# Kernel tuning notes

Measured on AMD Instinct MI355X. Metric: run time of the kernel, lower is better.

The kernel has to match this reference:

```python
import jax, jax.numpy as jnp
import numpy as np

EPS = 1e-5
NUM_GROUPS = 32

def _nin(x, w, b):
    # 1x1 conv: x (B,C,H,W), w (K,C), b (K,)
    return jnp.einsum('bchw,kc->bkhw', x, w) + b[None, :, None, None]

def _group_norm(x, gamma, beta, num_groups=NUM_GROUPS, eps=EPS):
    B, C, H, W = x.shape
    xg = x.reshape(B, num_groups, C // num_groups, H, W)
    mean = xg.mean(axis=(2, 3, 4), keepdims=True)
    var = xg.var(axis=(2, 3, 4), keepdims=True)
    xg = (xg - mean) * jax.lax.rsqrt(var + eps)
    x = xg.reshape(B, C, H, W)
    return x * gamma[None, :, None, None] + beta[None, :, None, None]

def setup_inputs() -> dict:
    key = jax.random.key(0)
    ks = jax.random.split(key, 10)
    B, C, H, W = 8, 512, 64, 64
    att = 512
    s = 0.02
    return {
        'x': jax.random.normal(ks[0], (B, C, H, W), dtype=jnp.float32),
        'gn_weight': jnp.ones((C,), jnp.float32),
        'gn_bias': jnp.zeros((C,), jnp.float32),
        'q_w': jax.random.normal(ks[1], (att, C), jnp.float32) * s,
        'q_b': jnp.zeros((att,), jnp.float32),
        'k_w': jax.random.normal(ks[2], (att, C), jnp.float32) * s,
        'k_b': jnp.zeros((att,), jnp.float32),
        'v_w': jax.random.normal(ks[3], (att, C), jnp.float32) * s,
        'v_b': jnp.zeros((att,), jnp.float32),
        'proj_w': jax.random.normal(ks[4], (C, att), jnp.float32) * s,
        'proj_b': jnp.zeros((C,), jnp.float32),
    }

def reference(x, gn_weight, gn_bias, q_w, q_b, k_w, k_b, v_w, v_b, proj_w, proj_b):
    B, C, H, W = x.shape
    h = _group_norm(x, gn_weight, gn_bias)
    q = _nin(h, q_w, q_b)  # (B, D, H, W)
    k = _nin(h, k_w, k_b)
    v = _nin(h, v_w, v_b)
    N = H * W
    qf = q.reshape(B, -1, N)
    kf = k.reshape(B, -1, N)
    vf = v.reshape(B, -1, N)
    scale = C ** (-0.5)  # note: scaled by input channel C, per source
    w = jnp.einsum('bdn,bdm->bnm', qf, kf) * scale  # (B, N, N)
    w = jax.nn.softmax(w, axis=-1)
    hf = jnp.einsum('bnm,bdm->bdn', w, vf)
    h = hf.reshape(B, -1, H, W)
    h = _nin(h, proj_w, proj_b)
    return x + h
```

## Files before the change

kernel.cpp:

```cpp
#include <hip/hip_runtime.h>
#include <hip/hip_bf16.h>
#include <cstdint>
#include <cstddef>

typedef __bf16 bf16_t;
typedef __bf16 bf16x8 __attribute__((ext_vector_type(8)));
typedef __bf16 bf16x4 __attribute__((ext_vector_type(4)));
typedef float f32x4 __attribute__((ext_vector_type(4)));

__device__ __forceinline__ void async16(const void* g, void* l) {
  __builtin_amdgcn_global_load_lds(
      (const __attribute__((address_space(1))) void*)g,
      (__attribute__((address_space(3))) void*)l,
      16, 0, 0);
}

__global__ __launch_bounds__(256) void f2b4(const float* __restrict__ w0,
                                            const float* __restrict__ w1,
                                            const float* __restrict__ w2,
                                            const float* __restrict__ w3,
                                            bf16_t* __restrict__ o0,
                                            bf16_t* __restrict__ o1,
                                            bf16_t* __restrict__ o2,
                                            bf16_t* __restrict__ o3) {
  const float* in = (blockIdx.y == 0) ? w0 : (blockIdx.y == 1) ? w1
                   : (blockIdx.y == 2) ? w2 : w3;
  bf16_t* out = (blockIdx.y == 0) ? o0 : (blockIdx.y == 1) ? o1
               : (blockIdx.y == 2) ? o2 : o3;
  const int i = blockIdx.x * 256 + threadIdx.x;
  float4 v = ((const float4*)in)[i];
  bf16x4 o = { (__bf16)v.x, (__bf16)v.y, (__bf16)v.z, (__bf16)v.w };
  ((bf16x4*)out)[i] = o;
}

__global__ __launch_bounds__(256) void groupnorm_t(const float* __restrict__ x,
                                                   const float* __restrict__ gamma,
                                                   const float* __restrict__ beta,
                                                   bf16_t* __restrict__ ht) {
  const int g = blockIdx.x;
  const int b = blockIdx.y;
  const int t = threadIdx.x;
  const float* xg = x + ((size_t)(b * 512 + g * 16)) * 4096;
  const float4* x4 = (const float4*)xg;

  float s = 0.f, ss = 0.f;
  #pragma unroll 8
  for (int i = t; i < 16384; i += 256) {
    float4 v = x4[i];
    s  += (v.x + v.y) + (v.z + v.w);
    ss += (v.x * v.x + v.y * v.y) + (v.z * v.z + v.w * v.w);
  }
  #pragma unroll
  for (int o = 32; o; o >>= 1) { s += __shfl_xor(s, o); ss += __shfl_xor(ss, o); }
  __shared__ float rs[4], rss[4];
  if ((t & 63) == 0) { rs[t >> 6] = s; rss[t >> 6] = ss; }
  __syncthreads();
  const float S  = (rs[0] + rs[1]) + (rs[2] + rs[3]);
  const float SS = (rss[0] + rss[1]) + (rss[2] + rss[3]);
  const float inv_n = 1.0f / 65536.0f;
  const float mean = S * inv_n;
  const float var  = SS * inv_n - mean * mean;
  const float rstd = rsqrtf(var + 1e-5f);

  float ga[16], be[16];
  #pragma unroll
  for (int cc = 0; cc < 16; cc++) {
    const float gm = gamma[g * 16 + cc] * rstd;
    ga[cc] = gm;
    be[cc] = beta[g * 16 + cc] - mean * gm;
  }

  bf16_t* hg = ht + (size_t)b * 4096 * 512 + g * 16;
  for (int n = t; n < 4096; n += 256) {
    bf16_t o[16];
    #pragma unroll
    for (int cc = 0; cc < 16; cc++)
      o[cc] = (bf16_t)(xg[(size_t)cc * 4096 + n] * ga[cc] + be[cc]);
    bf16x8* dst = (bf16x8*)(hg + (size_t)n * 512);
    dst[0] = *(bf16x8*)&o[0];
    dst[1] = *(bf16x8*)&o[8];
  }
}

template <int OUTF32, int BIAS_MODE, int RESID, int SWAP>
__global__ __launch_bounds__(256)
void gemm_bt(const bf16_t* __restrict__ A, const bf16_t* __restrict__ B,
             void* __restrict__ Cv, const float* __restrict__ bias,
             const float* __restrict__ resid,
             int TM, int TN, int Z, int K, float scale,
             long sA, long sB, long sC, long sR) {
  __shared__ alignas(16) bf16_t lA[4096];
  __shared__ alignas(16) bf16_t lB[4096];

  const int lid = blockIdx.x;
  const int xcd = lid & 7;
  const int j   = lid >> 3;
  const int sd  = SWAP ? TN : TM;
  const int I   = SWAP ? TM : TN;
  const int spx = (sd * Z) >> 3;
  const int strip = xcd * spx + j / I;
  const int inner = j % I;
  const int z    = strip / sd;
  const int sidx = strip % sd;
  const int bm = (SWAP ? inner : sidx) * 128;
  const int bn = (SWAP ? sidx : inner) * 128;
  const int N = TN * 128;

  const int t = threadIdx.x;
  const int lane = t & 63;
  const int w = t >> 6;
  const int wm = (w >> 1) * 64;
  const int wn = (w & 1) * 64;
  const bf16_t* Ab = A + (size_t)z * (size_t)sA;
  const bf16_t* Bb = B + (size_t)z * (size_t)sB;

  const int lrow = lane >> 2;
  const int lcol = (lane & 3) * 8;
  const int quad = lane >> 4;
  const int l15 = lane & 15;

  const bf16_t* gA0 = Ab + (size_t)(bm + w * 16 + lrow) * K + lcol;
  const bf16_t* gA1 = Ab + (size_t)(bm + (w + 4) * 16 + lrow) * K + lcol;
  const bf16_t* gB0 = Bb + (size_t)(bn + w * 16 + lrow) * K + lcol;
  const bf16_t* gB1 = Bb + (size_t)(bn + (w + 4) * 16 + lrow) * K + lcol;
  bf16_t* lA0 = &lA[w * 512];
  bf16_t* lA1 = &lA[(w + 4) * 512];
  bf16_t* lB0 = &lB[w * 512];
  bf16_t* lB1 = &lB[(w + 4) * 512];

  f32x4 acc[4][4] = {};

  for (int k0 = 0; k0 < K; k0 += 32) {
    __syncthreads();
    async16(gA0 + k0, lA0);
    async16(gA1 + k0, lA1);
    async16(gB0 + k0, lB0);
    async16(gB1 + k0, lB1);
    __syncthreads();

    bf16x8 af[4], bfr[4];
    #pragma unroll
    for (int i = 0; i < 4; i++) {
      af[i]  = *(const bf16x8*)&lA[(wm + i * 16 + l15) * 32 + quad * 8];
      bfr[i] = *(const bf16x8*)&lB[(wn + i * 16 + l15) * 32 + quad * 8];
    }
    #pragma unroll
    for (int i = 0; i < 4; i++)
      #pragma unroll
      for (int jj = 0; jj < 4; jj++)
        acc[i][jj] = __builtin_amdgcn_mfma_f32_16x16x32_bf16(af[i], bfr[jj],
                                                             acc[i][jj], 0, 0, 0);
  }

  float* Cf = (float*)Cv + (size_t)z * (size_t)sC;
  bf16_t* Cb = (bf16_t*)Cv + (size_t)z * (size_t)sC;
  const float* Rb = RESID ? (resid + (size_t)z * (size_t)sR) : nullptr;

  #pragma unroll
  for (int i = 0; i < 4; i++) {
    const int row0 = bm + wm + i * 16 + quad * 4;
    #pragma unroll
    for (int jj = 0; jj < 4; jj++) {
      const int col = bn + wn + jj * 16 + l15;
      #pragma unroll
      for (int r = 0; r < 4; r++) {
        float v = acc[i][jj][r] * scale;
        const int row = row0 + r;
        if (BIAS_MODE == 1) v += bias[row];
        else if (BIAS_MODE == 2) v += bias[col];
        const size_t idx = (size_t)row * N + col;
        if (RESID) v += Rb[idx];
        if (OUTF32) Cf[idx] = v;
        else Cb[idx] = (bf16_t)v;
      }
    }
  }
}

__global__ __launch_bounds__(512, 2)
void flash_attn(const bf16_t* __restrict__ Qm, const bf16_t* __restrict__ Km,
                const bf16_t* __restrict__ Vm, bf16_t* __restrict__ Om,
                float scale) {
  __shared__ alignas(16) bf16_t lT[2][4][128][32];
  __shared__ alignas(16) bf16_t lS[8][16][144];

  const int bid = blockIdx.x;
  const int z = bid & 7;
  const int qb = bid >> 3;
  const int m0 = qb * 128;

  const int t = threadIdx.x;
  const int lane = t & 63;
  const int w = t >> 6;
  const int quad = lane >> 4;
  const int l15 = lane & 15;
  const int srow = lane >> 2;
  const int scol = (lane & 3) * 8;

  const size_t sND = 4096ull * 512;
  const bf16_t* q = Qm + z * sND;
  const bf16_t* k = Km + z * sND;
  const bf16_t* v = Vm + z * sND;

  const bf16_t* kStage = k + (size_t)(w * 16 + srow) * 512 + scol;
  const bf16_t* vStage = v + (size_t)(w * 16 + srow) * 4096 + scol;

  bf16x8 qf[16];
  {
    const bf16_t* qrow = q + (size_t)(m0 + w * 16 + l15) * 512 + quad * 8;
    #pragma unroll
    for (int kk = 0; kk < 16; kk++)
      qf[kk] = *(const bf16x8*)(qrow + kk * 32);
  }

  f32x4 o_acc[32] = {};
  float l_run[4] = {0.f, 0.f, 0.f, 0.f};
  f32x4 s_acc[8];

  auto stageA = [&](int BUF, int kcc, int kd2) __attribute__((always_inline)) {
    #pragma unroll
    for (int c = 0; c < 4; c++)
      async16(kStage + (size_t)kcc * 512 + kd2 * 128 + c * 32,
              &lT[BUF][c][w * 16][0]);
  };
  auto stageC = [&](int BUF, int kcc, int db) __attribute__((always_inline)) {
    #pragma unroll
    for (int c = 0; c < 4; c++)
      async16(vStage + (size_t)db * 128 * 4096 + kcc + c * 32,
              &lT[BUF][c][w * 16][0]);
  };
  auto computeA = [&](int BUF, int kd2) __attribute__((always_inline)) {
    #pragma unroll
    for (int p = 0; p < 4; p++)
      #pragma unroll
      for (int n = 0; n < 8; n++) {
        bf16x8 kf = *(const bf16x8*)&lT[BUF][p][n * 16 + l15][quad * 8];
        s_acc[n] = __builtin_amdgcn_mfma_f32_16x16x32_bf16(
            qf[kd2 * 4 + p], kf, s_acc[n], 0, 0, 0);
      }
  };
  auto computeC = [&](int BUF, int db) __attribute__((always_inline)) {
    #pragma unroll
    for (int p = 0; p < 4; p++) {
      bf16x8 af = *(const bf16x8*)&lS[w][l15][p * 32 + quad * 8];
      #pragma unroll
      for (int nd = 0; nd < 8; nd++) {
        bf16x8 vf = *(const bf16x8*)&lT[BUF][p][nd * 16 + l15][quad * 8];
        o_acc[db * 8 + nd] = __builtin_amdgcn_mfma_f32_16x16x32_bf16(
            af, vf, o_acc[db * 8 + nd], 0, 0, 0);
      }
    }
  };
  auto phaseB = [&]() __attribute__((always_inline)) {
    float lsum[4] = {0.f, 0.f, 0.f, 0.f};
    #pragma unroll
    for (int n = 0; n < 8; n++)
      #pragma unroll
      for (int r = 0; r < 4; r++) {
        float e = __expf(s_acc[n][r] * scale);
        lsum[r] += e;
        lS[w][quad * 4 + r][n * 16 + l15] = (bf16_t)e;
      }
    #pragma unroll
    for (int r = 0; r < 4; r++) {
      float s = lsum[r];
      s += __shfl_xor(s, 1); s += __shfl_xor(s, 2);
      s += __shfl_xor(s, 4); s += __shfl_xor(s, 8);
      l_run[r] += s;
    }
  };

  stageA(0, 0, 0);
  __syncthreads();

  for (int kc = 0; kc < 4096; kc += 128) {
    #pragma unroll
    for (int n = 0; n < 8; n++) s_acc[n] = (f32x4){0.f, 0.f, 0.f, 0.f};

    stageA(1, kc, 1);  computeA(0, 0);            __syncthreads();
    stageA(0, kc, 2);  computeA(1, 1);            __syncthreads();
    stageA(1, kc, 3);  computeA(0, 2);            __syncthreads();
    stageC(0, kc, 0);  computeA(1, 3);  phaseB(); __syncthreads();
    stageC(1, kc, 1);  computeC(0, 0);            __syncthreads();
    stageC(0, kc, 2);  computeC(1, 1);            __syncthreads();
    stageC(1, kc, 3);  computeC(0, 2);            __syncthreads();
    if (kc + 128 < 4096) stageA(0, kc + 128, 0);
    computeC(1, 3);                               __syncthreads();
  }

  bf16_t* o = Om + z * sND;
  float rl[4];
  #pragma unroll
  for (int r = 0; r < 4; r++) rl[r] = 1.0f / l_run[r];
  #pragma unroll
  for (int nd = 0; nd < 32; nd++)
    #pragma unroll
    for (int r = 0; r < 4; r++) {
      const int row = m0 + w * 16 + quad * 4 + r;
      const int col = nd * 16 + l15;
      o[(size_t)row * 512 + col] = (bf16_t)(o_acc[nd][r] * rl[r]);
    }
}

extern "C" void kernel_launch(void* const* d_in, const int* in_sizes, int n_in,
                              void* d_out, int out_size, void* d_ws, size_t ws_size,
                              hipStream_t stream) {
  const float* x   = (const float*)d_in[0];
  const float* gnw = (const float*)d_in[1];
  const float* gnb = (const float*)d_in[2];
  const float* qw  = (const float*)d_in[3];
  const float* qb  = (const float*)d_in[4];
  const float* kw  = (const float*)d_in[5];
  const float* kb  = (const float*)d_in[6];
  const float* vw  = (const float*)d_in[7];
  const float* vb  = (const float*)d_in[8];
  const float* pw  = (const float*)d_in[9];
  const float* pb  = (const float*)d_in[10];
  float* out = (float*)d_out;

  char* ws = (char*)d_ws;
  size_t off = 0;
  auto alloc = [&](size_t bytes) -> void* {
    void* p = ws + off;
    off += (bytes + 255) & ~(size_t)255;
    return p;
  };

  const long sND = 4096L * 512;

  bf16_t* wqb = (bf16_t*)alloc(512ull * 512 * 2);
  bf16_t* wkb = (bf16_t*)alloc(512ull * 512 * 2);
  bf16_t* wvb = (bf16_t*)alloc(512ull * 512 * 2);
  bf16_t* wpb = (bf16_t*)alloc(512ull * 512 * 2);
  bf16_t* ht  = (bf16_t*)alloc(8ull * 4096 * 512 * 2);
  bf16_t* qbf = (bf16_t*)alloc(8ull * 4096 * 512 * 2);
  bf16_t* kbf = (bf16_t*)alloc(8ull * 4096 * 512 * 2);
  bf16_t* vbf = (bf16_t*)alloc(8ull * 4096 * 512 * 2);
  bf16_t* hfb = ht;

  f2b4<<<dim3(256, 4), 256, 0, stream>>>(qw, kw, vw, pw, wqb, wkb, wvb, wpb);
  groupnorm_t<<<dim3(32, 8), 256, 0, stream>>>(x, gnw, gnb, ht);

  gemm_bt<0, 2, 0, 0><<<1024, 256, 0, stream>>>(
      ht, wqb, qbf, qb, nullptr, 32, 4, 8, 512, 1.0f, sND, 0, sND, 0);
  gemm_bt<0, 2, 0, 0><<<1024, 256, 0, stream>>>(
      ht, wkb, kbf, kb, nullptr, 32, 4, 8, 512, 1.0f, sND, 0, sND, 0);
  gemm_bt<0, 1, 0, 1><<<1024, 256, 0, stream>>>(
      wvb, ht, vbf, vb, nullptr, 4, 32, 8, 512, 1.0f, 0, sND, sND, 0);

  const float scale = 0.044194173824159216f;
  flash_attn<<<256, 512, 0, stream>>>(qbf, kbf, vbf, hfb, scale);

  gemm_bt<1, 1, 1, 1><<<1024, 256, 0, stream>>>(
      wpb, hfb, out, pb, x, 4, 32, 8, 512, 1.0f, 0, sND, 512L * 4096, 512L * 4096);
}
```

Before: 701.8 us.

## Triple-buffer flash attention K/V staging with prefetch distance two and setprio

The LDS staging buffer grows from two to three slots so async global-to-LDS loads run two stages ahead of compute. Each stage now waits with a partial vmcnt plus a raw barrier instead of a full __syncthreads. The loop is unrolled in groups of three chunks so buffer indices stay compile-time constants. MFMA sections are also wrapped in s_setprio to favour math waves. The cost is more LDS per block, which may reduce occupancy, and fragile hand-counted vmcnt ordering.

```diff
diff --git a/kernel.cpp b/kernel.cpp
--- a/kernel.cpp
+++ b/kernel.cpp
@@ -181,7 +181,7 @@
 void flash_attn(const bf16_t* __restrict__ Qm, const bf16_t* __restrict__ Km,
                 const bf16_t* __restrict__ Vm, bf16_t* __restrict__ Om,
                 float scale) {
-  __shared__ alignas(16) bf16_t lT[2][4][128][32];
+  __shared__ alignas(16) bf16_t lT[3][4][128][32];
   __shared__ alignas(16) bf16_t lS[8][16][144];
 
   const int bid = blockIdx.x;
@@ -212,6 +212,7 @@
     for (int kk = 0; kk < 16; kk++)
       qf[kk] = *(const bf16x8*)(qrow + kk * 32);
   }
+  asm volatile("s_waitcnt vmcnt(0)" ::: "memory");
 
   f32x4 o_acc[32] = {};
   float l_run[4] = {0.f, 0.f, 0.f, 0.f};
@@ -230,6 +231,7 @@
               &lT[BUF][c][w * 16][0]);
   };
   auto computeA = [&](int BUF, int kd2) __attribute__((always_inline)) {
+    __builtin_amdgcn_s_setprio(1);
     #pragma unroll
     for (int p = 0; p < 4; p++)
       #pragma unroll
@@ -238,8 +240,10 @@
         s_acc[n] = __builtin_amdgcn_mfma_f32_16x16x32_bf16(
             qf[kd2 * 4 + p], kf, s_acc[n], 0, 0, 0);
       }
+    __builtin_amdgcn_s_setprio(0);
   };
   auto computeC = [&](int BUF, int db) __attribute__((always_inline)) {
+    __builtin_amdgcn_s_setprio(1);
     #pragma unroll
     for (int p = 0; p < 4; p++) {
       bf16x8 af = *(const bf16x8*)&lS[w][l15][p * 32 + quad * 8];
@@ -250,6 +254,7 @@
             af, vf, o_acc[db * 8 + nd], 0, 0, 0);
       }
     }
+    __builtin_amdgcn_s_setprio(0);
   };
   auto phaseB = [&]() __attribute__((always_inline)) {
     float lsum[4] = {0.f, 0.f, 0.f, 0.f};
@@ -269,24 +274,48 @@
       l_run[r] += s;
     }
   };
+  auto slotWB = [&]() __attribute__((always_inline)) {
+    asm volatile("s_waitcnt vmcnt(4)" ::: "memory");
+    __builtin_amdgcn_s_barrier();
+    __builtin_amdgcn_sched_barrier(0);
+  };
+
+  auto chunk = [&](int kc, int PH) __attribute__((always_inline)) {
+    const int kcn = (kc + 128) & 4095;
+    #pragma unroll
+    for (int j = 0; j < 8; j++) {
+      const int BUF  = (PH + j) % 3;
+      const int SBUF = (PH + j + 2) % 3;
+      slotWB();
+      if (j + 2 < 4)      stageA(SBUF, kc, j + 2);
+      else if (j + 2 < 8) stageC(SBUF, kc, j + 2 - 4);
+      else                stageA(SBUF, kcn, j + 2 - 8);
+      __builtin_amdgcn_sched_barrier(0);
+      if (j < 4) {
+        if (j == 0) {
+          #pragma unroll
+          for (int n = 0; n < 8; n++) s_acc[n] = (f32x4){0.f, 0.f, 0.f, 0.f};
+        }
+        computeA(BUF, j);
+        if (j == 3) phaseB();
+      } else {
+        computeC(BUF, j - 4);
+      }
+    }
+  };
 
   stageA(0, 0, 0);
-  __syncthreads();
-
-  for (int kc = 0; kc < 4096; kc += 128) {
-    #pragma unroll
-    for (int n = 0; n < 8; n++) s_acc[n] = (f32x4){0.f, 0.f, 0.f, 0.f};
-
-    stageA(1, kc, 1);  computeA(0, 0);            __syncthreads();
-    stageA(0, kc, 2);  computeA(1, 1);            __syncthreads();
-    stageA(1, kc, 3);  computeA(0, 2);            __syncthreads();
-    stageC(0, kc, 0);  computeA(1, 3);  phaseB(); __syncthreads();
-    stageC(1, kc, 1);  computeC(0, 0);            __syncthreads();
-    stageC(0, kc, 2);  computeC(1, 1);            __syncthreads();
-    stageC(1, kc, 3);  computeC(0, 2);            __syncthreads();
-    if (kc + 128 < 4096) stageA(0, kc + 128, 0);
-    computeC(1, 3);                               __syncthreads();
-  }
+  stageA(1, 0, 1);
+
+  for (int kc = 0; kc < 3840; kc += 384) {
+    chunk(kc, 0);
+    chunk(kc + 128, 2);
+    chunk(kc + 256, 1);
+  }
+  chunk(3840, 0);
+  chunk(3968, 2);
+
+  asm volatile("s_waitcnt vmcnt(0)" ::: "memory");
 
   bf16_t* o = Om + z * sND;
   float rl[4];
```

Result: slower. 1.025 ms (+46.1%).

## Pair waves in PV stage to share V fragments across two row blocks

Applied to the files above, without the earlier changes.

Changes the P·V MFMA work split so each pair of waves covers two 16-row softmax tiles and splits the D columns in half. Each V fragment loaded from LDS now feeds two MFMAs, halving V LDS reads per wave, while the P fragments read doubles. Row normalizers are exchanged through a small shared array before the output write. LDS traffic in the PV phase drops, at the cost of an extra barrier and a reshuffled output mapping.

```diff
diff --git a/kernel.cpp b/kernel.cpp
--- a/kernel.cpp
+++ b/kernel.cpp
@@ -183,6 +183,7 @@
                 float scale) {
   __shared__ alignas(16) bf16_t lT[2][4][128][32];
   __shared__ alignas(16) bf16_t lS[8][16][144];
+  __shared__ float lL[8][16];
 
   const int bid = blockIdx.x;
   const int z = bid & 7;
@@ -196,6 +197,8 @@
   const int l15 = lane & 15;
   const int srow = lane >> 2;
   const int scol = (lane & 3) * 8;
+  const int g2 = w & 6;
+  const int dh = w & 1;
 
   const size_t sND = 4096ull * 512;
   const bf16_t* q = Qm + z * sND;
@@ -242,12 +245,15 @@
   auto computeC = [&](int BUF, int db) __attribute__((always_inline)) {
     #pragma unroll
     for (int p = 0; p < 4; p++) {
-      bf16x8 af = *(const bf16x8*)&lS[w][l15][p * 32 + quad * 8];
-      #pragma unroll
-      for (int nd = 0; nd < 8; nd++) {
-        bf16x8 vf = *(const bf16x8*)&lT[BUF][p][nd * 16 + l15][quad * 8];
+      bf16x8 af0 = *(const bf16x8*)&lS[g2][l15][p * 32 + quad * 8];
+      bf16x8 af1 = *(const bf16x8*)&lS[g2 + 1][l15][p * 32 + quad * 8];
+      #pragma unroll
+      for (int nd = 0; nd < 4; nd++) {
+        bf16x8 vf = *(const bf16x8*)&lT[BUF][p][dh * 64 + nd * 16 + l15][quad * 8];
         o_acc[db * 8 + nd] = __builtin_amdgcn_mfma_f32_16x16x32_bf16(
-            af, vf, o_acc[db * 8 + nd], 0, 0, 0);
+            af0, vf, o_acc[db * 8 + nd], 0, 0, 0);
+        o_acc[db * 8 + 4 + nd] = __builtin_amdgcn_mfma_f32_16x16x32_bf16(
+            af1, vf, o_acc[db * 8 + 4 + nd], 0, 0, 0);
       }
     }
   };
@@ -288,18 +294,31 @@
     computeC(1, 3);                               __syncthreads();
   }
 
+  if (l15 == 0) {
+    #pragma unroll
+    for (int r = 0; r < 4; r++) lL[w][quad * 4 + r] = l_run[r];
+  }
+  __syncthreads();
+  float rl[2][4];
+  #pragma unroll
+  for (int s = 0; s < 2; s++)
+    #pragma unroll
+    for (int r = 0; r < 4; r++) rl[s][r] = 1.0f / lL[g2 + s][quad * 4 + r];
+
   bf16_t* o = Om + z * sND;
-  float rl[4];
-  #pragma unroll
-  for (int r = 0; r < 4; r++) rl[r] = 1.0f / l_run[r];
-  #pragma unroll
-  for (int nd = 0; nd < 32; nd++)
-    #pragma unroll
-    for (int r = 0; r < 4; r++) {
-      const int row = m0 + w * 16 + quad * 4 + r;
-      const int col = nd * 16 + l15;
-      o[(size_t)row * 512 + col] = (bf16_t)(o_acc[nd][r] * rl[r]);
-    }
+  #pragma unroll
+  for (int db = 0; db < 4; db++)
+    #pragma unroll
+    for (int s = 0; s < 2; s++)
+      #pragma unroll
+      for (int nd = 0; nd < 4; nd++)
+        #pragma unroll
+        for (int r = 0; r < 4; r++) {
+          const int row = m0 + (g2 + s) * 16 + quad * 4 + r;
+          const int col = db * 128 + dh * 64 + nd * 16 + l15;
+          o[(size_t)row * 512 + col] =
+              (bf16_t)(o_acc[db * 8 + s * 4 + nd][r] * rl[s][r]);
+        }
 }
 
 extern "C" void kernel_launch(void* const* d_in, const int* in_sizes, int n_in,
```

Result: faster. 661.4 us (-5.8%).
